# Kernel tuning notes

Hardware: AMD Instinct MI355X
Metric: run time of the kernel (lower is better)

Reference implementation:

```python
import jax, jax.numpy as jnp
import numpy as np

MAX_LEN = 2048

def setup_inputs() -> dict:
    key = jax.random.key(0)
    k1, k2, k3 = jax.random.split(key, 3)
    B, S, E, V, C = 32, 2048, 512, 50257, 2
    x = jax.random.randint(k1, (B, S), 0, V, dtype=jnp.int64)
    emb_table = jax.random.normal(k2, (V, E), dtype=jnp.float32) * 0.02
    fc_w = jax.random.normal(k3, (C, E), dtype=jnp.float32) * 0.02
    fc_b = jnp.zeros((C,), dtype=jnp.float32)
    return {"x": x, "emb_table": emb_table, "fc_w": fc_w, "fc_b": fc_b}

def reference(x, emb_table, fc_w, fc_b):
    x = x[:, :MAX_LEN]                               # [B,S]
    x_emb = emb_table[x]                             # [B,S,E]
    scores = jnp.einsum('bse,bte->bst', x_emb, x_emb)  # [B,S,S] unscaled
    attn = jax.nn.softmax(scores, axis=-1)
    attended = jnp.einsum('bst,bte->bse', attn, x_emb)  # [B,S,E]
    pooled = attended.max(axis=1)                    # pool='max' -> [B,E]
    return pooled @ fc_w.T + fc_b                    # [B,C]
```

## Files before the change

kernel.cpp:

```cpp
#include <hip/hip_runtime.h>
#include <float.h>


typedef __attribute__((ext_vector_type(8))) short short8;
typedef __attribute__((ext_vector_type(4))) float f32x4;
typedef __attribute__((ext_vector_type(16))) float f32x16;
typedef __attribute__((ext_vector_type(4))) short s16x4;

__device__ __forceinline__ short f2bf(float f) {
  unsigned u = __float_as_uint(f);
  unsigned r = (u + 0x7fffu + ((u >> 16) & 1u)) >> 16;
  return (short)r;
}
__device__ __forceinline__ unsigned ordf(float f) {
  unsigned u = __float_as_uint(f);
  return (u & 0x80000000u) ? ~u : (u | 0x80000000u);
}
__device__ __forceinline__ float unordf(unsigned e) {
  unsigned u = (e & 0x80000000u) ? (e ^ 0x80000000u) : ~e;
  return __uint_as_float(u);
}
__device__ __forceinline__ void gload16(const void* g, void* s) {
  __builtin_amdgcn_global_load_lds((const __attribute__((address_space(1))) void*)g,
                                   (__attribute__((address_space(3))) void*)s,
                                   16, 0, 0);
}
__device__ __forceinline__ unsigned pkbf(float lo, float hi) {
  unsigned r;
  asm("v_cvt_pk_bf16_f32 %0, %1, %2" : "=v"(r) : "v"(lo), "v"(hi));
  return r;
}
#define PLSWAP(a, b) asm volatile("v_permlane32_swap_b32 %0, %1" : "+v"(a), "+v"(b))

extern "C" __global__ __launch_bounds__(256)
void prep3(const int* __restrict__ xp, const float* __restrict__ emb,
           short* __restrict__ Kf, short* __restrict__ Vf) {
  __shared__ __align__(16) short ls[32 * 520];
  const int t = threadIdx.x, kt = blockIdx.x, b = blockIdx.y;
  {
    const int r = t >> 3, seg = t & 7;
    const float* src = emb + (long)xp[b * 2048 + kt * 32 + r] * 512 + seg * 64;
    short* ldst = ls + r * 520 + seg * 64;
#pragma unroll
    for (int i = 0; i < 8; ++i) {
      float4 fa = *(const float4*)(src + i * 8);
      float4 fb = *(const float4*)(src + i * 8 + 4);
      short8 v = { f2bf(fa.x), f2bf(fa.y), f2bf(fa.z), f2bf(fa.w),
                   f2bf(fb.x), f2bf(fb.y), f2bf(fb.z), f2bf(fb.w) };
      *(short8*)(ldst + i * 8) = v;
    }
  }
  __syncthreads();
#pragma unroll
  for (int rr = 0; rr < 8; ++rr) {
    int j = rr * 256 + t;
    int s = j >> 6, l = j & 63;
    int q32 = l & 31, hi = l >> 5;
    short8 v = *(const short8*)(ls + q32 * 520 + s * 16 + hi * 8);
    *(short8*)(Kf + ((long)(b * 2048 + kt * 32 + s) * 64 + l) * 8) = v;
  }
#pragma unroll
  for (int rr = 0; rr < 8; ++rr) {
    int j = rr * 256 + t;
    int eb = j >> 7, ks2 = (j >> 6) & 1, l = j & 63;
    int e32 = l & 31, hi = l >> 5;
    const short* colp = ls + (ks2 * 16 + hi * 8) * 520 + eb * 32 + e32;
    short8 v = { colp[0], colp[520], colp[1040], colp[1560],
                 colp[2080], colp[2600], colp[3120], colp[3640] };
    *(short8*)(Vf + ((long)(b * 2048 + eb * 128 + kt * 2 + ks2) * 64 + l) * 8) = v;
  }
}

extern "C" __global__ __launch_bounds__(512, 2)
void attn5(const short* __restrict__ Kf, const short* __restrict__ Vf,
           unsigned* __restrict__ pooled) {
  __shared__ __align__(16) uint4 lq4[64 * 64];
  __shared__ __align__(16) uint4 lp4[2][32 * 64];
  __shared__ float lsm[512];

  const int t = threadIdx.x, l = t & 63, w = t >> 6;
  const int n = blockIdx.x;
  const int b = (n & 7) + ((n >> 8) << 3);
  const int qt = (n >> 3) & 31;
  const int q32 = l & 31, hi = l >> 5;
  const short* lqs = (const short*)lq4;

  {
    const short* src = Kf + (long)(b * 2048 + qt * 64) * 512;
#pragma unroll
    for (int i = 0; i < 8; ++i) {
      int sw = i * 512 + w * 64;
      gload16(src + (long)(sw + l) * 8, lq4 + sw);
    }
  }

  const short* kp0 = Kf + ((long)(b * 2048 + w * 32) * 64 + l) * 8;
  const short* vp0 = Vf + ((long)(b * 2048 + (2 * w) * 128) * 64 + l) * 8;

#define LOADK(dst, base, sb)                                                  \
  {                                                                           \
    _Pragma("unroll") for (int i = 0; i < 8; ++i)                             \
        dst[i] = *(const short8*)((base) + ((sb) * 8 + i) * 512);             \
  }
#define MFMAK(src, sb)                                                        \
  {                                                                           \
    _Pragma("unroll") for (int i = 0; i < 8; ++i) {                           \
      int s = (sb) * 8 + i;                                                   \
      short8 qv0 = *(const short8*)(lqs + (s * 64 + l) * 8);                  \
      short8 qv1 = *(const short8*)(lqs + ((32 + s) * 64 + l) * 8);           \
      S0 = __builtin_amdgcn_mfma_f32_32x32x16_bf16(src[i], qv0, S0, 0, 0, 0); \
      S1 = __builtin_amdgcn_mfma_f32_32x32x16_bf16(src[i], qv1, S1, 0, 0, 0); \
    }                                                                         \
  }

  short8 kA[8], kB[8];
  LOADK(kA, kp0, 0)
  LOADK(kB, kp0, 1)
  __syncthreads();

  f32x16 acc[2][2];
#pragma unroll
  for (int eg = 0; eg < 2; ++eg)
#pragma unroll
    for (int qg = 0; qg < 2; ++qg)
#pragma unroll
      for (int r = 0; r < 16; ++r) acc[eg][qg][r] = 0.f;
  float lr0 = 0.f, lr1 = 0.f;
  int buf = 0;

  for (int kt = 0; kt < 8; ++kt) {
    const short* kp = kp0 + (long)(kt * 256) * 512;
    f32x16 S0, S1;
#pragma unroll
    for (int r = 0; r < 16; ++r) { S0[r] = 0.f; S1[r] = 0.f; }
    __builtin_amdgcn_s_setprio(1);
    MFMAK(kA, 0)
    __builtin_amdgcn_s_setprio(0);
    LOADK(kA, kp, 2)
    __builtin_amdgcn_s_setprio(1);
    MFMAK(kB, 1)
    __builtin_amdgcn_s_setprio(0);
    LOADK(kB, kp, 3)
    __builtin_amdgcn_s_setprio(1);
    MFMAK(kA, 2)
    MFMAK(kB, 3)
    __builtin_amdgcn_s_setprio(0);

    float ps0 = 0.f, ps1 = 0.f;
#pragma unroll
    for (int r = 0; r < 16; ++r) {
      S0[r] = __expf(S0[r]); ps0 += S0[r];
      S1[r] = __expf(S1[r]); ps1 += S1[r];
    }
    lr0 += ps0; lr1 += ps1;

    const short* vp = vp0 + (long)(kt * 16) * 512;
    short8 vb[8];
#pragma unroll
    for (int ks = 0; ks < 4; ++ks) {
      vb[2 * ks]     = *(const short8*)(vp + ks * 512);
      vb[2 * ks + 1] = *(const short8*)(vp + 128 * 512 + ks * 512);
    }
    if (kt < 7) {
      const short* kp2 = kp0 + (long)((kt + 1) * 256) * 512;
      LOADK(kA, kp2, 0)
      LOADK(kB, kp2, 1)
    }

    {
      unsigned a0 = pkbf(S0[0], S0[1]),   c0 = pkbf(S0[4], S0[5]);   PLSWAP(a0, c0);
      unsigned a1 = pkbf(S0[2], S0[3]),   c1 = pkbf(S0[6], S0[7]);   PLSWAP(a1, c1);
      unsigned a2 = pkbf(S0[8], S0[9]),   c2 = pkbf(S0[12], S0[13]); PLSWAP(a2, c2);
      unsigned a3 = pkbf(S0[10], S0[11]), c3 = pkbf(S0[14], S0[15]); PLSWAP(a3, c3);
      lp4[buf][(4 * w + 0) * 64 + l] = (uint4){a0, a1, c0, c1};
      lp4[buf][(4 * w + 2) * 64 + l] = (uint4){a2, a3, c2, c3};
      unsigned d0 = pkbf(S1[0], S1[1]),   e0 = pkbf(S1[4], S1[5]);   PLSWAP(d0, e0);
      unsigned d1 = pkbf(S1[2], S1[3]),   e1 = pkbf(S1[6], S1[7]);   PLSWAP(d1, e1);
      unsigned d2 = pkbf(S1[8], S1[9]),   e2 = pkbf(S1[12], S1[13]); PLSWAP(d2, e2);
      unsigned d3 = pkbf(S1[10], S1[11]), e3 = pkbf(S1[14], S1[15]); PLSWAP(d3, e3);
      lp4[buf][(4 * w + 1) * 64 + l] = (uint4){d0, d1, e0, e1};
      lp4[buf][(4 * w + 3) * 64 + l] = (uint4){d2, d3, e2, e3};
    }
    asm volatile("s_waitcnt lgkmcnt(0)" ::: "memory");
    __builtin_amdgcn_s_barrier();

    const short* lps = (const short*)lp4[buf];
#pragma unroll
    for (int ks = 0; ks < 16; ++ks) {
      short8 v0 = vb[(ks & 3) * 2];
      short8 v1 = vb[(ks & 3) * 2 + 1];
      short8 pf0 = *(const short8*)(lps + ((ks * 2 + 0) * 64 + l) * 8);
      short8 pf1 = *(const short8*)(lps + ((ks * 2 + 1) * 64 + l) * 8);
      __builtin_amdgcn_s_setprio(1);
      acc[0][0] = __builtin_amdgcn_mfma_f32_32x32x16_bf16(v0, pf0, acc[0][0], 0, 0, 0);
      acc[0][1] = __builtin_amdgcn_mfma_f32_32x32x16_bf16(v0, pf1, acc[0][1], 0, 0, 0);
      acc[1][0] = __builtin_amdgcn_mfma_f32_32x32x16_bf16(v1, pf0, acc[1][0], 0, 0, 0);
      acc[1][1] = __builtin_amdgcn_mfma_f32_32x32x16_bf16(v1, pf1, acc[1][1], 0, 0, 0);
      __builtin_amdgcn_s_setprio(0);
      if (ks < 12) {
        vb[(ks & 3) * 2]     = *(const short8*)(vp + (ks + 4) * 512);
        vb[(ks & 3) * 2 + 1] = *(const short8*)(vp + 128 * 512 + (ks + 4) * 512);
      }
    }
    buf ^= 1;
  }

  lr0 += __shfl_xor(lr0, 32, 64);
  lr1 += __shfl_xor(lr1, 32, 64);
  __syncthreads();
  if (l < 32) {
    lsm[w * 32 + l] = lr0;
    lsm[256 + w * 32 + l] = lr1;
  }
  __syncthreads();
  float lt0 = lsm[q32], lt1 = lsm[256 + q32];
#pragma unroll
  for (int kg = 1; kg < 8; ++kg) {
    lt0 += lsm[kg * 32 + q32];
    lt1 += lsm[256 + kg * 32 + q32];
  }
  float ri0 = 1.0f / lt0, ri1 = 1.0f / lt1;
#pragma unroll
  for (int eg = 0; eg < 2; ++eg)
#pragma unroll
    for (int r = 0; r < 16; ++r) {
      float v = fmaxf(acc[eg][0][r] * ri0, acc[eg][1][r] * ri1);
      v = fmaxf(v, __shfl_xor(v, 1, 64));
      v = fmaxf(v, __shfl_xor(v, 2, 64));
      v = fmaxf(v, __shfl_xor(v, 4, 64));
      v = fmaxf(v, __shfl_xor(v, 8, 64));
      v = fmaxf(v, __shfl_xor(v, 16, 64));
      if (q32 == 0) {
        int e = (2 * w + eg) * 32 + (r & 3) + 8 * (r >> 2) + 4 * hi;
        atomicMax(&pooled[b * 512 + e], ordf(v));
      }
    }
}

#define LDKp 520
#define LDVp 40
#define LDPp 40
extern "C" __global__ __launch_bounds__(256, 2)
void attn_fb(const int* __restrict__ xp, const float* __restrict__ emb,
             unsigned* __restrict__ pooled) {
  __shared__ __align__(16) short lds_k[32 * LDKp];
  __shared__ __align__(16) short lds_vt[512 * LDVp];
  __shared__ __align__(16) short lds_p[64 * LDPp];
  const int t = threadIdx.x, l = t & 63, w = t >> 6;
  const int b = blockIdx.y;
  const int q0 = blockIdx.x * 64;
  const int L = l & 15, g = l >> 4;
  short8 qf[16];
  {
    int qq = q0 + w * 16 + L;
    const float* qrow = emb + (long)xp[b * 2048 + qq] * 512;
#pragma unroll
    for (int ec = 0; ec < 16; ++ec) {
      int e0 = ec * 32 + 8 * g;
      float4 fa = *(const float4*)(qrow + e0);
      float4 fb = *(const float4*)(qrow + e0 + 4);
      short8 v = { f2bf(fa.x), f2bf(fa.y), f2bf(fa.z), f2bf(fa.w),
                   f2bf(fb.x), f2bf(fb.y), f2bf(fb.z), f2bf(fb.w) };
      qf[ec] = v;
    }
  }
  f32x4 acc[32];
#pragma unroll
  for (int nt = 0; nt < 32; ++nt) acc[nt] = (f32x4){0.f, 0.f, 0.f, 0.f};
  float mrun[4] = {-FLT_MAX, -FLT_MAX, -FLT_MAX, -FLT_MAX};
  float lrun[4] = {0.f, 0.f, 0.f, 0.f};
  for (int kt = 0; kt < 64; ++kt) {
    __syncthreads();
    if (t < 128) {
#pragma unroll 4
      for (int i = 0; i < 32; ++i) {
        const float* krow = emb + (long)xp[b * 2048 + kt * 32 + i] * 512;
        float4 f = *(const float4*)(krow + 4 * t);
        s16x4 v = { f2bf(f.x), f2bf(f.y), f2bf(f.z), f2bf(f.w) };
        *(s16x4*)&lds_k[i * LDKp + 4 * t] = v;
      }
    } else {
      const int u = t - 128, lane_ = u & 63, half = u >> 6;
#pragma unroll 2
      for (int kq = 0; kq < 8; ++kq) {
        const int kbase = b * 2048 + kt * 32 + kq * 4;
        const float* r0 = emb + (long)xp[kbase + 0] * 512;
        const float* r1 = emb + (long)xp[kbase + 1] * 512;
        const float* r2 = emb + (long)xp[kbase + 2] * 512;
        const float* r3 = emb + (long)xp[kbase + 3] * 512;
#pragma unroll
        for (int seg = 0; seg < 4; ++seg) {
          int e = lane_ + 64 * (seg + 4 * half);
          s16x4 v = { f2bf(r0[e]), f2bf(r1[e]), f2bf(r2[e]), f2bf(r3[e]) };
          *(s16x4*)&lds_vt[e * LDVp + 4 * kq] = v;
        }
      }
    }
    __syncthreads();
    f32x4 s0 = {0.f, 0.f, 0.f, 0.f}, s1 = {0.f, 0.f, 0.f, 0.f};
#pragma unroll
    for (int ec = 0; ec < 16; ++ec) {
      short8 k0 = *(const short8*)&lds_k[L * LDKp + ec * 32 + 8 * g];
      short8 k1 = *(const short8*)&lds_k[(L + 16) * LDKp + ec * 32 + 8 * g];
      s0 = __builtin_amdgcn_mfma_f32_16x16x32_bf16(qf[ec], k0, s0, 0, 0, 0);
      s1 = __builtin_amdgcn_mfma_f32_16x16x32_bf16(qf[ec], k1, s1, 0, 0, 0);
    }
    float p0[4], p1[4], sc[4];
#pragma unroll
    for (int r = 0; r < 4; ++r) {
      float v = fmaxf(s0[r], s1[r]);
      v = fmaxf(v, __shfl_xor(v, 1, 64));
      v = fmaxf(v, __shfl_xor(v, 2, 64));
      v = fmaxf(v, __shfl_xor(v, 4, 64));
      v = fmaxf(v, __shfl_xor(v, 8, 64));
      float nm = fmaxf(mrun[r], v);
      sc[r] = expf(mrun[r] - nm);
      p0[r] = expf(s0[r] - nm);
      p1[r] = expf(s1[r] - nm);
      float rs = p0[r] + p1[r];
      rs += __shfl_xor(rs, 1, 64);
      rs += __shfl_xor(rs, 2, 64);
      rs += __shfl_xor(rs, 4, 64);
      rs += __shfl_xor(rs, 8, 64);
      lrun[r] = lrun[r] * sc[r] + rs;
      mrun[r] = nm;
    }
    if (__any(sc[0] < 1.f || sc[1] < 1.f || sc[2] < 1.f || sc[3] < 1.f)) {
      f32x4 sv = { sc[0], sc[1], sc[2], sc[3] };
#pragma unroll
      for (int nt = 0; nt < 32; ++nt) acc[nt] *= sv;
    }
#pragma unroll
    for (int r = 0; r < 4; ++r) {
      int row = w * 16 + g * 4 + r;
      lds_p[row * LDPp + L]      = f2bf(p0[r]);
      lds_p[row * LDPp + 16 + L] = f2bf(p1[r]);
    }
    asm volatile("s_waitcnt lgkmcnt(0)" ::: "memory");
    short8 pf = *(const short8*)&lds_p[(w * 16 + L) * LDPp + 8 * g];
#pragma unroll
    for (int nt = 0; nt < 32; ++nt) {
      short8 vf = *(const short8*)&lds_vt[(nt * 16 + L) * LDVp + 8 * g];
      acc[nt] = __builtin_amdgcn_mfma_f32_16x16x32_bf16(pf, vf, acc[nt], 0, 0, 0);
    }
  }
  __syncthreads();
  float inv[4];
#pragma unroll
  for (int r = 0; r < 4; ++r) inv[r] = 1.f / lrun[r];
  float* rbuf = (float*)lds_k;
#pragma unroll
  for (int nt = 0; nt < 32; ++nt) {
    f32x4 a = acc[nt];
    float c = fmaxf(fmaxf(a[0] * inv[0], a[1] * inv[1]),
                    fmaxf(a[2] * inv[2], a[3] * inv[3]));
    c = fmaxf(c, __shfl_xor(c, 16, 64));
    c = fmaxf(c, __shfl_xor(c, 32, 64));
    if (g == 0) rbuf[w * 512 + nt * 16 + L] = c;
  }
  __syncthreads();
  for (int j = t; j < 512; j += 256) {
    float v = fmaxf(fmaxf(rbuf[j], rbuf[512 + j]),
                    fmaxf(rbuf[1024 + j], rbuf[1536 + j]));
    atomicMax(&pooled[b * 512 + j], ordf(v));
  }
}

extern "C" __global__ void fc_small(const unsigned* __restrict__ pooled,
                                    const float* __restrict__ fw,
                                    const float* __restrict__ fb,
                                    float* __restrict__ out) {
  int t = threadIdx.x;
  if (t >= 64) return;
  int bb = t >> 1, c = t & 1;
  float s = fb[c];
  for (int e = 0; e < 512; ++e)
    s += unordf(pooled[bb * 512 + e]) * fw[c * 512 + e];
  out[t] = s;
}

extern "C" void kernel_launch(void* const* d_in, const int* in_sizes, int n_in,
                              void* d_out, int out_size, void* d_ws, size_t ws_size,
                              hipStream_t stream) {
  const int* xp    = (const int*)d_in[0];
  const float* emb = (const float*)d_in[1];
  const float* fw  = (const float*)d_in[2];
  const float* fb  = (const float*)d_in[3];
  unsigned* pooled = (unsigned*)d_ws;

  hipMemsetAsync(pooled, 0, 32 * 512 * sizeof(unsigned), stream);

  const size_t need = 65536ull + 2ull * 33554432ull * sizeof(short);
  if (ws_size >= need) {
    short* Kff = (short*)((char*)d_ws + 65536);
    short* Vff = Kff + 33554432;
    prep3<<<dim3(64, 32), 256, 0, stream>>>(xp, emb, Kff, Vff);
    attn5<<<dim3(1024), 512, 0, stream>>>(Kff, Vff, pooled);
  } else {
    attn_fb<<<dim3(32, 32), 256, 0, stream>>>(xp, emb, pooled);
  }
  fc_small<<<1, 64, 0, stream>>>(pooled, fw, fb, (float*)d_out);
}
```

Baseline: 344.6 us.

## Warp-specialize attention: producer waves compute QK softmax, consumer waves do PV

Splits the 8 waves of the attention block into 4 producer waves that compute the QK^T scores, exponentiate and write bf16 probabilities to double-buffered LDS, and 4 consumer waves that run the PV MFMAs and the max-pooling. The goal is to overlap the score and exp work with the PV matrix multiplies across waves instead of serialising them within each wave. In exchange the producers and consumers must stay in lockstep through matched s_barrier counts, each wave holds more registers (acc[4][2] on consumers), and the MFMA work is now split unevenly between the two roles. An unused attn6 variant that never writes pooled is also left in the file.

After: 357.8 us. 1.04x slower.

```diff
diff --git a/kernel.cpp b/kernel.cpp
--- a/kernel.cpp
+++ b/kernel.cpp
@@ -72,11 +72,11 @@
 }
 
 extern "C" __global__ __launch_bounds__(512, 2)
-void attn5(const short* __restrict__ Kf, const short* __restrict__ Vf,
+void attn6(const short* __restrict__ Kf, const short* __restrict__ Vf,
            unsigned* __restrict__ pooled) {
   __shared__ __align__(16) uint4 lq4[64 * 64];
   __shared__ __align__(16) uint4 lp4[2][32 * 64];
-  __shared__ float lsm[512];
+  __shared__ float lsm[256];
 
   const int t = threadIdx.x, l = t & 63, w = t >> 6;
   const int n = blockIdx.x;
@@ -94,147 +94,282 @@
     }
   }
 
-  const short* kp0 = Kf + ((long)(b * 2048 + w * 32) * 64 + l) * 8;
-  const short* vp0 = Vf + ((long)(b * 2048 + (2 * w) * 128) * 64 + l) * 8;
-
-#define LOADK(dst, base, sb)                                                  \
+#define PLOADP(d0, d1, p0, p1, off)                                           \
   {                                                                           \
-    _Pragma("unroll") for (int i = 0; i < 8; ++i)                             \
-        dst[i] = *(const short8*)((base) + ((sb) * 8 + i) * 512);             \
-  }
-#define MFMAK(src, sb)                                                        \
+    _Pragma("unroll") for (int i = 0; i < 4; ++i) {                           \
+      d0[i] = *(const short8*)((p0) + (off) + i * 512);                       \
+      d1[i] = *(const short8*)((p1) + (off) + i * 512);                       \
+    }                                                                         \
+  }
+#define PMFMA(s0_, s1_, ch)                                                   \
   {                                                                           \
-    _Pragma("unroll") for (int i = 0; i < 8; ++i) {                           \
-      int s = (sb) * 8 + i;                                                   \
+    __builtin_amdgcn_s_setprio(1);                                            \
+    _Pragma("unroll") for (int i = 0; i < 4; ++i) {                           \
+      int s = (ch) * 4 + i;                                                   \
       short8 qv0 = *(const short8*)(lqs + (s * 64 + l) * 8);                  \
       short8 qv1 = *(const short8*)(lqs + ((32 + s) * 64 + l) * 8);           \
-      S0 = __builtin_amdgcn_mfma_f32_32x32x16_bf16(src[i], qv0, S0, 0, 0, 0); \
-      S1 = __builtin_amdgcn_mfma_f32_32x32x16_bf16(src[i], qv1, S1, 0, 0, 0); \
+      S00 = __builtin_amdgcn_mfma_f32_32x32x16_bf16(s0_[i], qv0, S00, 0, 0, 0); \
+      S01 = __builtin_amdgcn_mfma_f32_32x32x16_bf16(s0_[i], qv1, S01, 0, 0, 0); \
+      S10 = __builtin_amdgcn_mfma_f32_32x32x16_bf16(s1_[i], qv0, S10, 0, 0, 0); \
+      S11 = __builtin_amdgcn_mfma_f32_32x32x16_bf16(s1_[i], qv1, S11, 0, 0, 0); \
     }                                                                         \
-  }
-
-  short8 kA[8], kB[8];
-  LOADK(kA, kp0, 0)
-  LOADK(kB, kp0, 1)
+    __builtin_amdgcn_s_setprio(0);                                            \
+  }
+#define PACK(Sq0, Sq1, sb, buf)                                               \
+  {                                                                           \
+    unsigned a0 = pkbf(Sq0[0], Sq0[1]),  c0 = pkbf(Sq0[4], Sq0[5]);  PLSWAP(a0, c0); \
+    unsigned a1 = pkbf(Sq0[2], Sq0[3]),  c1 = pkbf(Sq0[6], Sq0[7]);  PLSWAP(a1, c1); \
+    unsigned a2 = pkbf(Sq0[8], Sq0[9]),  c2 = pkbf(Sq0[12], Sq0[13]); PLSWAP(a2, c2); \
+    unsigned a3 = pkbf(Sq0[10], Sq0[11]), c3 = pkbf(Sq0[14], Sq0[15]); PLSWAP(a3, c3); \
+    lp4[buf][((sb) + 0) * 64 + l] = (uint4){a0, a1, c0, c1};                  \
+    lp4[buf][((sb) + 2) * 64 + l] = (uint4){a2, a3, c2, c3};                  \
+    unsigned d0 = pkbf(Sq1[0], Sq1[1]),  e0 = pkbf(Sq1[4], Sq1[5]);  PLSWAP(d0, e0); \
+    unsigned d1 = pkbf(Sq1[2], Sq1[3]),  e1 = pkbf(Sq1[6], Sq1[7]);  PLSWAP(d1, e1); \
+    unsigned d2 = pkbf(Sq1[8], Sq1[9]),  e2 = pkbf(Sq1[12], Sq1[13]); PLSWAP(d2, e2); \
+    unsigned d3 = pkbf(Sq1[10], Sq1[11]), e3 = pkbf(Sq1[14], Sq1[15]); PLSWAP(d3, e3); \
+    lp4[buf][((sb) + 1) * 64 + l] = (uint4){d0, d1, e0, e1};                  \
+    lp4[buf][((sb) + 3) * 64 + l] = (uint4){d2, d3, e2, e3};                  \
+  }
+
+  if (w < 4) {
+    const short* kb0 = Kf + (long)(b * 2048 + (2 * w + 0) * 32) * 512 + l * 8;
+    const short* kb1 = Kf + (long)(b * 2048 + (2 * w + 1) * 32) * 512 + l * 8;
+    short8 kA0[4], kA1[4], kB0[4], kB1[4];
+    PLOADP(kA0, kA1, kb0, kb1, 0)
+    PLOADP(kB0, kB1, kb0, kb1, 2048)
+    float lr0 = 0.f, lr1 = 0.f;
+    __syncthreads();
+
+    for (int kt = 0; kt < 8; ++kt) {
+      const short* kp0 = kb0 + (long)kt * 131072;
+      const short* kp1 = kb1 + (long)kt * 131072;
+      const long nxt = (kt < 7) ? 131072 : 0;
+      f32x16 S00, S01, S10, S11;
+#pragma unroll
+      for (int r = 0; r < 16; ++r) { S00[r] = 0.f; S01[r] = 0.f; S10[r] = 0.f; S11[r] = 0.f; }
+      PMFMA(kA0, kA1, 0) PLOADP(kA0, kA1, kp0, kp1, 2 * 2048)
+      PMFMA(kB0, kB1, 1) PLOADP(kB0, kB1, kp0, kp1, 3 * 2048)
+      PMFMA(kA0, kA1, 2) PLOADP(kA0, kA1, kp0, kp1, 4 * 2048)
+      PMFMA(kB0, kB1, 3) PLOADP(kB0, kB1, kp0, kp1, 5 * 2048)
+      PMFMA(kA0, kA1, 4) PLOADP(kA0, kA1, kp0, kp1, 6 * 2048)
+      PMFMA(kB0, kB1, 5) PLOADP(kB0, kB1, kp0, kp1, 7 * 2048)
+      PMFMA(kA0, kA1, 6) PLOADP(kA0, kA1, kp0, kp1, nxt)
+      PMFMA(kB0, kB1, 7) PLOADP(kB0, kB1, kp0, kp1, nxt + 2048)
+
+      float ps0 = 0.f, ps1 = 0.f;
+#pragma unroll
+      for (int r = 0; r < 16; ++r) {
+        S00[r] = __expf(S00[r]); ps0 += S00[r];
+        S01[r] = __expf(S01[r]); ps1 += S01[r];
+        S10[r] = __expf(S10[r]); ps0 += S10[r];
+        S11[r] = __expf(S11[r]); ps1 += S11[r];
+      }
+      lr0 += ps0; lr1 += ps1;
+
+      const int buf = kt & 1;
+      PACK(S00, S01, 8 * w, buf)
+      PACK(S10, S11, 8 * w + 4, buf)
+      asm volatile("s_waitcnt lgkmcnt(0)" ::: "memory");
+      __builtin_amdgcn_s_barrier();
+    }
+    __builtin_amdgcn_s_barrier();
+
+    lr0 += __shfl_xor(lr0, 32, 64);
+    lr1 += __shfl_xor(lr1, 32, 64);
+    if (l < 32) {
+      lsm[w * 32 + l] = lr0;
+      lsm[128 + w * 32 + l] = lr1;
+    }
+  } else {
+    const int wc = w - 4;
+    const short* vp0 = Vf + (long)(b * 2048 + (4 * wc + 0) * 128) * 512 + l * 8;
+    const short* vp1 = Vf + (long)(b * 2048 + (4 * wc + 1) * 128) * 512 + l * 8;
+    const short* vp2 = Vf + (long)(b * 2048 + (4 * wc + 2) * 128) * 512 + l * 8;
+    const short* vp3 = Vf + (long)(b * 2048 + (4 * wc + 3) * 128) * 512 + l * 8;
+    f32x16 acc[4][2];
+#pragma unroll
+    for (int g = 0; g < 4; ++g)
+#pragma unroll
+      for (int qg = 0; qg < 2; ++qg)
+#pragma unroll
+        for (int r = 0; r < 16; ++r) acc[g][qg][r] = 0.f;
+    short8 vbA[4], vbB[4];
+    vbA[0] = *(const short8*)(vp0); vbA[1] = *(const short8*)(vp1);
+    vbA[2] = *(const short8*)(vp2); vbA[3] = *(const short8*)(vp3);
+    vbB[0] = *(const short8*)(vp0 + 512); vbB[1] = *(const short8*)(vp1 + 512);
+    vbB[2] = *(const short8*)(vp2 + 512); vbB[3] = *(const short8*)(vp3 + 512);
+    __syncthreads();
+    __builtin_amdgcn_s_barrier();
+
+#define CSTEP(ks_, ring)                                                      \
+  {                                                                           \
+    short8 pf0 = *(const short8*)(lps + ((2 * (ks_)) * 64 + l) * 8);          \
+    short8 pf1 = *(const short8*)(lps + ((2 * (ks_) + 1) * 64 + l) * 8);      \
+    __builtin_amdgcn_s_setprio(1);                                            \
+    _Pragma("unroll") for (int g = 0; g < 4; ++g) {                           \
+      acc[g][0] = __builtin_amdgcn_mfma_f32_32x32x16_bf16(ring[g], pf0, acc[g][0], 0, 0, 0); \
+      acc[g][1] = __builtin_amdgcn_mfma_f32_32x32x16_bf16(ring[g], pf1, acc[g][1], 0, 0, 0); \
+    }                                                                         \
+    __builtin_amdgcn_s_setprio(0);                                            \
+    {                                                                         \
+      const int nk = (ksg0 + (ks_) + 2) & 127;                                \
+      ring[0] = *(const short8*)(vp0 + (long)nk * 512);                       \
+      ring[1] = *(const short8*)(vp1 + (long)nk * 512);                       \
+      ring[2] = *(const short8*)(vp2 + (long)nk * 512);                       \
+      ring[3] = *(const short8*)(vp3 + (long)nk * 512);                       \
+    }                                                                         \
+  }
+
+    for (int kt = 1; kt <= 8; ++kt) {
+      const short* lps = (const short*)lp4[(kt - 1) & 1];
+      const int ksg0 = (kt - 1) * 16;
+#pragma unroll
+      for (int ks2 = 0; ks2 < 8; ++ks2) {
+        CSTEP(2 * ks2, vbA)
+        CSTEP(2 * ks2 + 1, vbB)
+      }
+      __builtin_amdgcn_s_barrier();
+    }
+
+    (void)0;
+  }
   __syncthreads();
 
-  f32x16 acc[2][2];
-#pragma unroll
-  for (int eg = 0; eg < 2; ++eg)
-#pragma unroll
-    for (int qg = 0; qg < 2; ++qg)
-#pragma unroll
-      for (int r = 0; r < 16; ++r) acc[eg][qg][r] = 0.f;
-  float lr0 = 0.f, lr1 = 0.f;
-  int buf = 0;
-
-  for (int kt = 0; kt < 8; ++kt) {
-    const short* kp = kp0 + (long)(kt * 256) * 512;
-    f32x16 S0, S1;
-#pragma unroll
-    for (int r = 0; r < 16; ++r) { S0[r] = 0.f; S1[r] = 0.f; }
-    __builtin_amdgcn_s_setprio(1);
-    MFMAK(kA, 0)
-    __builtin_amdgcn_s_setprio(0);
-    LOADK(kA, kp, 2)
-    __builtin_amdgcn_s_setprio(1);
-    MFMAK(kB, 1)
-    __builtin_amdgcn_s_setprio(0);
-    LOADK(kB, kp, 3)
-    __builtin_amdgcn_s_setprio(1);
-    MFMAK(kA, 2)
-    MFMAK(kB, 3)
-    __builtin_amdgcn_s_setprio(0);
-
-    float ps0 = 0.f, ps1 = 0.f;
-#pragma unroll
-    for (int r = 0; r < 16; ++r) {
-      S0[r] = __expf(S0[r]); ps0 += S0[r];
-      S1[r] = __expf(S1[r]); ps1 += S1[r];
-    }
-    lr0 += ps0; lr1 += ps1;
-
-    const short* vp = vp0 + (long)(kt * 16) * 512;
-    short8 vb[8];
-#pragma unroll
-    for (int ks = 0; ks < 4; ++ks) {
-      vb[2 * ks]     = *(const short8*)(vp + ks * 512);
-      vb[2 * ks + 1] = *(const short8*)(vp + 128 * 512 + ks * 512);
-    }
-    if (kt < 7) {
-      const short* kp2 = kp0 + (long)((kt + 1) * 256) * 512;
-      LOADK(kA, kp2, 0)
-      LOADK(kB, kp2, 1)
-    }
-
-    {
-      unsigned a0 = pkbf(S0[0], S0[1]),   c0 = pkbf(S0[4], S0[5]);   PLSWAP(a0, c0);
-      unsigned a1 = pkbf(S0[2], S0[3]),   c1 = pkbf(S0[6], S0[7]);   PLSWAP(a1, c1);
-      unsigned a2 = pkbf(S0[8], S0[9]),   c2 = pkbf(S0[12], S0[13]); PLSWAP(a2, c2);
-      unsigned a3 = pkbf(S0[10], S0[11]), c3 = pkbf(S0[14], S0[15]); PLSWAP(a3, c3);
-      lp4[buf][(4 * w + 0) * 64 + l] = (uint4){a0, a1, c0, c1};
-      lp4[buf][(4 * w + 2) * 64 + l] = (uint4){a2, a3, c2, c3};
-      unsigned d0 = pkbf(S1[0], S1[1]),   e0 = pkbf(S1[4], S1[5]);   PLSWAP(d0, e0);
-      unsigned d1 = pkbf(S1[2], S1[3]),   e1 = pkbf(S1[6], S1[7]);   PLSWAP(d1, e1);
-      unsigned d2 = pkbf(S1[8], S1[9]),   e2 = pkbf(S1[12], S1[13]); PLSWAP(d2, e2);
-      unsigned d3 = pkbf(S1[10], S1[11]), e3 = pkbf(S1[14], S1[15]); PLSWAP(d3, e3);
-      lp4[buf][(4 * w + 1) * 64 + l] = (uint4){d0, d1, e0, e1};
-      lp4[buf][(4 * w + 3) * 64 + l] = (uint4){d2, d3, e2, e3};
-    }
-    asm volatile("s_waitcnt lgkmcnt(0)" ::: "memory");
+  if (w >= 4) {
+    const int wc = w - 4;
+    float lt0 = lsm[q32] + lsm[32 + q32] + lsm[64 + q32] + lsm[96 + q32];
+    float lt1 = lsm[128 + q32] + lsm[160 + q32] + lsm[192 + q32] + lsm[224 + q32];
+    float ri0 = 1.0f / lt0, ri1 = 1.0f / lt1;
+    (void)ri0; (void)ri1; (void)wc;
+  }
+}
+
+
+extern "C" __global__ __launch_bounds__(512, 2)
+void attn6b(const short* __restrict__ Kf, const short* __restrict__ Vf,
+            unsigned* __restrict__ pooled) {
+  __shared__ __align__(16) uint4 lq4[64 * 64];
+  __shared__ __align__(16) uint4 lp4[2][32 * 64];
+  __shared__ float lsm[256];
+
+  const int t = threadIdx.x, l = t & 63, w = t >> 6;
+  const int n = blockIdx.x;
+  const int b = (n & 7) + ((n >> 8) << 3);
+  const int qt = (n >> 3) & 31;
+  const int q32 = l & 31, hi = l >> 5;
+  const short* lqs = (const short*)lq4;
+
+  {
+    const short* src = Kf + (long)(b * 2048 + qt * 64) * 512;
+#pragma unroll
+    for (int i = 0; i < 8; ++i) {
+      int sw = i * 512 + w * 64;
+      gload16(src + (long)(sw + l) * 8, lq4 + sw);
+    }
+  }
+
+  if (w < 4) {
+    const short* kb0 = Kf + (long)(b * 2048 + (2 * w + 0) * 32) * 512 + l * 8;
+    const short* kb1 = Kf + (long)(b * 2048 + (2 * w + 1) * 32) * 512 + l * 8;
+    short8 kA0[4], kA1[4], kB0[4], kB1[4];
+    PLOADP(kA0, kA1, kb0, kb1, 0)
+    PLOADP(kB0, kB1, kb0, kb1, 2048)
+    float lr0 = 0.f, lr1 = 0.f;
+    __syncthreads();
+
+    for (int kt = 0; kt < 8; ++kt) {
+      const short* kp0 = kb0 + (long)kt * 131072;
+      const short* kp1 = kb1 + (long)kt * 131072;
+      const long nxt = (kt < 7) ? 131072 : 0;
+      f32x16 S00, S01, S10, S11;
+#pragma unroll
+      for (int r = 0; r < 16; ++r) { S00[r] = 0.f; S01[r] = 0.f; S10[r] = 0.f; S11[r] = 0.f; }
+      PMFMA(kA0, kA1, 0) PLOADP(kA0, kA1, kp0, kp1, 2 * 2048)
+      PMFMA(kB0, kB1, 1) PLOADP(kB0, kB1, kp0, kp1, 3 * 2048)
+      PMFMA(kA0, kA1, 2) PLOADP(kA0, kA1, kp0, kp1, 4 * 2048)
+      PMFMA(kB0, kB1, 3) PLOADP(kB0, kB1, kp0, kp1, 5 * 2048)
+      PMFMA(kA0, kA1, 4) PLOADP(kA0, kA1, kp0, kp1, 6 * 2048)
+      PMFMA(kB0, kB1, 5) PLOADP(kB0, kB1, kp0, kp1, 7 * 2048)
+      PMFMA(kA0, kA1, 6) PLOADP(kA0, kA1, kp0, kp1, nxt)
+      PMFMA(kB0, kB1, 7) PLOADP(kB0, kB1, kp0, kp1, nxt + 2048)
+
+      float ps0 = 0.f, ps1 = 0.f;
+#pragma unroll
+      for (int r = 0; r < 16; ++r) {
+        S00[r] = __expf(S00[r]); ps0 += S00[r];
+        S01[r] = __expf(S01[r]); ps1 += S01[r];
+        S10[r] = __expf(S10[r]); ps0 += S10[r];
+        S11[r] = __expf(S11[r]); ps1 += S11[r];
+      }
+      lr0 += ps0; lr1 += ps1;
+
+      const int buf = kt & 1;
+      PACK(S00, S01, 8 * w, buf)
+      PACK(S10, S11, 8 * w + 4, buf)
+      asm volatile("s_waitcnt lgkmcnt(0)" ::: "memory");
+      __builtin_amdgcn_s_barrier();
+    }
     __builtin_amdgcn_s_barrier();
 
-    const short* lps = (const short*)lp4[buf];
-#pragma unroll
-    for (int ks = 0; ks < 16; ++ks) {
-      short8 v0 = vb[(ks & 3) * 2];
-      short8 v1 = vb[(ks & 3) * 2 + 1];
-      short8 pf0 = *(const short8*)(lps + ((ks * 2 + 0) * 64 + l) * 8);
-      short8 pf1 = *(const short8*)(lps + ((ks * 2 + 1) * 64 + l) * 8);
-      __builtin_amdgcn_s_setprio(1);
-      acc[0][0] = __builtin_amdgcn_mfma_f32_32x32x16_bf16(v0, pf0, acc[0][0], 0, 0, 0);
-      acc[0][1] = __builtin_amdgcn_mfma_f32_32x32x16_bf16(v0, pf1, acc[0][1], 0, 0, 0);
-      acc[1][0] = __builtin_amdgcn_mfma_f32_32x32x16_bf16(v1, pf0, acc[1][0], 0, 0, 0);
-      acc[1][1] = __builtin_amdgcn_mfma_f32_32x32x16_bf16(v1, pf1, acc[1][1], 0, 0, 0);
-      __builtin_amdgcn_s_setprio(0);
-      if (ks < 12) {
-        vb[(ks & 3) * 2]     = *(const short8*)(vp + (ks + 4) * 512);
-        vb[(ks & 3) * 2 + 1] = *(const short8*)(vp + 128 * 512 + (ks + 4) * 512);
-      }
-    }
-    buf ^= 1;
-  }
-
-  lr0 += __shfl_xor(lr0, 32, 64);
-  lr1 += __shfl_xor(lr1, 32, 64);
-  __syncthreads();
-  if (l < 32) {
-    lsm[w * 32 + l] = lr0;
-    lsm[256 + w * 32 + l] = lr1;
-  }
-  __syncthreads();
-  float lt0 = lsm[q32], lt1 = lsm[256 + q32];
-#pragma unroll
-  for (int kg = 1; kg < 8; ++kg) {
-    lt0 += lsm[kg * 32 + q32];
-    lt1 += lsm[256 + kg * 32 + q32];
-  }
-  float ri0 = 1.0f / lt0, ri1 = 1.0f / lt1;
-#pragma unroll
-  for (int eg = 0; eg < 2; ++eg)
-#pragma unroll
-    for (int r = 0; r < 16; ++r) {
-      float v = fmaxf(acc[eg][0][r] * ri0, acc[eg][1][r] * ri1);
-      v = fmaxf(v, __shfl_xor(v, 1, 64));
-      v = fmaxf(v, __shfl_xor(v, 2, 64));
-      v = fmaxf(v, __shfl_xor(v, 4, 64));
-      v = fmaxf(v, __shfl_xor(v, 8, 64));
-      v = fmaxf(v, __shfl_xor(v, 16, 64));
-      if (q32 == 0) {
-        int e = (2 * w + eg) * 32 + (r & 3) + 8 * (r >> 2) + 4 * hi;
-        atomicMax(&pooled[b * 512 + e], ordf(v));
-      }
-    }
+    lr0 += __shfl_xor(lr0, 32, 64);
+    lr1 += __shfl_xor(lr1, 32, 64);
+    if (l < 32) {
+      lsm[w * 32 + l] = lr0;
+      lsm[128 + w * 32 + l] = lr1;
+    }
+    __syncthreads();
+  } else {
+    const int wc = w - 4;
+    const short* vp0 = Vf + (long)(b * 2048 + (4 * wc + 0) * 128) * 512 + l * 8;
+    const short* vp1 = Vf + (long)(b * 2048 + (4 * wc + 1) * 128) * 512 + l * 8;
+    const short* vp2 = Vf + (long)(b * 2048 + (4 * wc + 2) * 128) * 512 + l * 8;
+    const short* vp3 = Vf + (long)(b * 2048 + (4 * wc + 3) * 128) * 512 + l * 8;
+    f32x16 acc[4][2];
+#pragma unroll
+    for (int g = 0; g < 4; ++g)
+#pragma unroll
+      for (int qg = 0; qg < 2; ++qg)
+#pragma unroll
+        for (int r = 0; r < 16; ++r) acc[g][qg][r] = 0.f;
+    short8 vbA[4], vbB[4];
+    vbA[0] = *(const short8*)(vp0); vbA[1] = *(const short8*)(vp1);
+    vbA[2] = *(const short8*)(vp2); vbA[3] = *(const short8*)(vp3);
+    vbB[0] = *(const short8*)(vp0 + 512); vbB[1] = *(const short8*)(vp1 + 512);
+    vbB[2] = *(const short8*)(vp2 + 512); vbB[3] = *(const short8*)(vp3 + 512);
+    __syncthreads();
+    __builtin_amdgcn_s_barrier();
+
+    for (int kt = 1; kt <= 8; ++kt) {
+      const short* lps = (const short*)lp4[(kt - 1) & 1];
+      const int ksg0 = (kt - 1) * 16;
+#pragma unroll
+      for (int ks2 = 0; ks2 < 8; ++ks2) {
+        CSTEP(2 * ks2, vbA)
+        CSTEP(2 * ks2 + 1, vbB)
+      }
+      __builtin_amdgcn_s_barrier();
+    }
+    __syncthreads();
+
+    float lt0 = lsm[q32] + lsm[32 + q32] + lsm[64 + q32] + lsm[96 + q32];
+    float lt1 = lsm[128 + q32] + lsm[160 + q32] + lsm[192 + q32] + lsm[224 + q32];
+    float ri0 = 1.0f / lt0, ri1 = 1.0f / lt1;
+#pragma unroll
+    for (int g = 0; g < 4; ++g)
+#pragma unroll
+      for (int r = 0; r < 16; ++r) {
+        float v = fmaxf(acc[g][0][r] * ri0, acc[g][1][r] * ri1);
+        v = fmaxf(v, __shfl_xor(v, 1, 64));
+        v = fmaxf(v, __shfl_xor(v, 2, 64));
+        v = fmaxf(v, __shfl_xor(v, 4, 64));
+        v = fmaxf(v, __shfl_xor(v, 8, 64));
+        v = fmaxf(v, __shfl_xor(v, 16, 64));
+        if (q32 == 0) {
+          int e = 128 * wc + 32 * g + (r & 3) + 8 * (r >> 2) + 4 * hi;
+          atomicMax(&pooled[b * 512 + e], ordf(v));
+        }
+      }
+  }
 }
 
 #define LDKp 520
@@ -395,7 +530,7 @@
     short* Kff = (short*)((char*)d_ws + 65536);
     short* Vff = Kff + 33554432;
     prep3<<<dim3(64, 32), 256, 0, stream>>>(xp, emb, Kff, Vff);
-    attn5<<<dim3(1024), 512, 0, stream>>>(Kff, Vff, pooled);
+    attn6b<<<dim3(1024), 512, 0, stream>>>(Kff, Vff, pooled);
   } else {
     attn_fb<<<dim3(32, 32), 256, 0, stream>>>(xp, emb, pooled);
   }
```

## Quantize Q/K to FP8 e4m3 and compute scores with FP8 MFMA

Applied to the files above, without the earlier changes.

The prep kernel now emits K (which also serves as Q) in FP8 e4m3 with a new packed layout, and the attention kernel computes QK^T with 32x32x16 fp8 MFMA instead of bf16. This halves K/Q memory traffic and LDS footprint and uses the higher-throughput FP8 matrix path. The K prefetch schedule is simplified so whole tiles are loaded ahead. The risk is reduced score precision: embeddings are ~0.02 scale, so many values fall into e4m3 subnormals or flush to zero, which could change the softmax output.

Result: faster. 310.7 us (-9.8%).

```diff
diff --git a/kernel.cpp b/kernel.cpp
--- a/kernel.cpp
+++ b/kernel.cpp
@@ -12,6 +12,31 @@
   unsigned r = (u + 0x7fffu + ((u >> 16) & 1u)) >> 16;
   return (short)r;
 }
+__device__ __forceinline__ float bf2f(short s) {
+  return __uint_as_float(((unsigned)(unsigned short)s) << 16);
+}
+__device__ __forceinline__ unsigned f2e4m3(float f) {
+  unsigned u = __float_as_uint(f);
+  unsigned s = (u >> 31) << 7;
+  int exp = (int)((u >> 23) & 0xff) - 127;
+  unsigned m = (u & 0x7fffff) | 0x800000;
+  if (exp < -10) return s;
+  int shift = 20, e4 = 0;
+  if (exp >= -6) e4 = exp + 7;
+  else shift += (-6 - exp);
+  unsigned keep = m >> shift;
+  unsigned rem = m & ((1u << shift) - 1u);
+  unsigned half = 1u << (shift - 1);
+  keep += (rem > half || (rem == half && (keep & 1)));
+  unsigned out;
+  if (e4 > 0) {
+    if (keep >= 16) { keep >>= 1; e4++; }
+    out = ((unsigned)e4 << 3) | (keep & 7);
+  } else {
+    out = (keep >= 8) ? ((1u << 3) | (keep & 7)) : keep;
+  }
+  return s | out;
+}
 __device__ __forceinline__ unsigned ordf(float f) {
   unsigned u = __float_as_uint(f);
   return (u & 0x80000000u) ? ~u : (u | 0x80000000u);
@@ -31,10 +56,13 @@
   return r;
 }
 #define PLSWAP(a, b) asm volatile("v_permlane32_swap_b32 %0, %1" : "+v"(a), "+v"(b))
+__device__ __forceinline__ long long mklong(unsigned lo, unsigned hi) {
+  return (long long)((((unsigned long long)hi) << 32) | lo);
+}
 
 extern "C" __global__ __launch_bounds__(256)
-void prep3(const int* __restrict__ xp, const float* __restrict__ emb,
-           short* __restrict__ Kf, short* __restrict__ Vf) {
+void prep4(const int* __restrict__ xp, const float* __restrict__ emb,
+           unsigned char* __restrict__ Kf8, short* __restrict__ Vf) {
   __shared__ __align__(16) short ls[32 * 520];
   const int t = threadIdx.x, kt = blockIdx.x, b = blockIdx.y;
   {
@@ -51,13 +79,28 @@
     }
   }
   __syncthreads();
-#pragma unroll
-  for (int rr = 0; rr < 8; ++rr) {
-    int j = rr * 256 + t;
-    int s = j >> 6, l = j & 63;
-    int q32 = l & 31, hi = l >> 5;
-    short8 v = *(const short8*)(ls + q32 * 520 + s * 16 + hi * 8);
-    *(short8*)(Kf + ((long)(b * 2048 + kt * 32 + s) * 64 + l) * 8) = v;
+  {
+    const long chunkK = ((long)b * 64 + kt) * 16384;
+#pragma unroll
+    for (int i = 0; i < 4; ++i) {
+      int j = t * 4 + i;
+      int sp = j >> 6, lj = j & 63;
+      int keyl = lj & 31, hi2 = lj >> 5;
+      const short* row = ls + keyl * 520 + 8 * hi2;
+      unsigned dw[4];
+#pragma unroll
+      for (int c2 = 0; c2 < 4; ++c2) {
+        unsigned d = 0;
+#pragma unroll
+        for (int bb2 = 0; bb2 < 4; ++bb2) {
+          int c = c2 * 4 + bb2;
+          int e = 16 * (2 * sp + (c >> 3)) + (c & 7);
+          d |= f2e4m3(bf2f(row[e])) << (8 * bb2);
+        }
+        dw[c2] = d;
+      }
+      *(uint4*)(Kf8 + chunkK + (long)j * 16) = (uint4){dw[0], dw[1], dw[2], dw[3]};
+    }
   }
 #pragma unroll
   for (int rr = 0; rr < 8; ++rr) {
@@ -72,9 +115,9 @@
 }
 
 extern "C" __global__ __launch_bounds__(512, 2)
-void attn5(const short* __restrict__ Kf, const short* __restrict__ Vf,
+void attn7(const unsigned char* __restrict__ Kf8, const short* __restrict__ Vf,
            unsigned* __restrict__ pooled) {
-  __shared__ __align__(16) uint4 lq4[64 * 64];
+  __shared__ __align__(16) uint4 lq8[32 * 64];
   __shared__ __align__(16) uint4 lp4[2][32 * 64];
   __shared__ float lsm[512];
 
@@ -83,39 +126,39 @@
   const int b = (n & 7) + ((n >> 8) << 3);
   const int qt = (n >> 3) & 31;
   const int q32 = l & 31, hi = l >> 5;
-  const short* lqs = (const short*)lq4;
 
   {
-    const short* src = Kf + (long)(b * 2048 + qt * 64) * 512;
-#pragma unroll
-    for (int i = 0; i < 8; ++i) {
+    const unsigned char* src = Kf8 + ((long)b * 64 + 2 * qt) * 16384;
+#pragma unroll
+    for (int i = 0; i < 4; ++i) {
       int sw = i * 512 + w * 64;
-      gload16(src + (long)(sw + l) * 8, lq4 + sw);
-    }
-  }
-
-  const short* kp0 = Kf + ((long)(b * 2048 + w * 32) * 64 + l) * 8;
+      gload16(src + (long)(sw + l) * 16, lq8 + sw);
+    }
+  }
+
+  const unsigned char* kc0 = Kf8 + ((long)b * 64 + w) * 16384 + (long)l * 16;
   const short* vp0 = Vf + ((long)(b * 2048 + (2 * w) * 128) * 64 + l) * 8;
 
-#define LOADK(dst, base, sb)                                                  \
+#define LOADK8(dst, base, half)                                               \
   {                                                                           \
     _Pragma("unroll") for (int i = 0; i < 8; ++i)                             \
-        dst[i] = *(const short8*)((base) + ((sb) * 8 + i) * 512);             \
-  }
-#define MFMAK(src, sb)                                                        \
+        dst[i] = *(const uint4*)((base) + ((half) * 8 + i) * 1024);           \
+  }
+#define QK8(kv, sp)                                                           \
   {                                                                           \
-    _Pragma("unroll") for (int i = 0; i < 8; ++i) {                           \
-      int s = (sb) * 8 + i;                                                   \
-      short8 qv0 = *(const short8*)(lqs + (s * 64 + l) * 8);                  \
-      short8 qv1 = *(const short8*)(lqs + ((32 + s) * 64 + l) * 8);           \
-      S0 = __builtin_amdgcn_mfma_f32_32x32x16_bf16(src[i], qv0, S0, 0, 0, 0); \
-      S1 = __builtin_amdgcn_mfma_f32_32x32x16_bf16(src[i], qv1, S1, 0, 0, 0); \
-    }                                                                         \
-  }
-
-  short8 kA[8], kB[8];
-  LOADK(kA, kp0, 0)
-  LOADK(kB, kp0, 1)
+    long long ak0 = mklong(kv.x, kv.y);                                       \
+    long long ak1 = mklong(kv.z, kv.w);                                       \
+    uint4 qa = lq8[(sp) * 64 + l];                                            \
+    uint4 qb = lq8[(16 + (sp)) * 64 + l];                                     \
+    S0 = __builtin_amdgcn_mfma_f32_32x32x16_fp8_fp8(ak0, mklong(qa.x, qa.y), S0, 0, 0, 0); \
+    S1 = __builtin_amdgcn_mfma_f32_32x32x16_fp8_fp8(ak0, mklong(qb.x, qb.y), S1, 0, 0, 0); \
+    S0 = __builtin_amdgcn_mfma_f32_32x32x16_fp8_fp8(ak1, mklong(qa.z, qa.w), S0, 0, 0, 0); \
+    S1 = __builtin_amdgcn_mfma_f32_32x32x16_fp8_fp8(ak1, mklong(qb.z, qb.w), S1, 0, 0, 0); \
+  }
+
+  uint4 kA[8], kB[8];
+  LOADK8(kA, kc0, 0)
+  LOADK8(kB, kc0, 1)
   __syncthreads();
 
   f32x16 acc[2][2];
@@ -129,21 +172,14 @@
   int buf = 0;
 
   for (int kt = 0; kt < 8; ++kt) {
-    const short* kp = kp0 + (long)(kt * 256) * 512;
     f32x16 S0, S1;
 #pragma unroll
     for (int r = 0; r < 16; ++r) { S0[r] = 0.f; S1[r] = 0.f; }
     __builtin_amdgcn_s_setprio(1);
-    MFMAK(kA, 0)
-    __builtin_amdgcn_s_setprio(0);
-    LOADK(kA, kp, 2)
-    __builtin_amdgcn_s_setprio(1);
-    MFMAK(kB, 1)
-    __builtin_amdgcn_s_setprio(0);
-    LOADK(kB, kp, 3)
-    __builtin_amdgcn_s_setprio(1);
-    MFMAK(kA, 2)
-    MFMAK(kB, 3)
+#pragma unroll
+    for (int sp = 0; sp < 8; ++sp) QK8(kA[sp], sp)
+#pragma unroll
+    for (int sp = 0; sp < 8; ++sp) QK8(kB[sp], 8 + sp)
     __builtin_amdgcn_s_setprio(0);
 
     float ps0 = 0.f, ps1 = 0.f;
@@ -161,10 +197,11 @@
       vb[2 * ks]     = *(const short8*)(vp + ks * 512);
       vb[2 * ks + 1] = *(const short8*)(vp + 128 * 512 + ks * 512);
     }
-    if (kt < 7) {
-      const short* kp2 = kp0 + (long)((kt + 1) * 256) * 512;
-      LOADK(kA, kp2, 0)
-      LOADK(kB, kp2, 1)
+    {
+      const int nkt = (kt < 7) ? kt + 1 : 7;
+      const unsigned char* kcn = kc0 + (long)nkt * 131072;
+      LOADK8(kA, kcn, 0)
+      LOADK8(kB, kcn, 1)
     }
 
     {
@@ -390,12 +427,12 @@
 
   hipMemsetAsync(pooled, 0, 32 * 512 * sizeof(unsigned), stream);
 
-  const size_t need = 65536ull + 2ull * 33554432ull * sizeof(short);
+  const size_t need = 65536ull + 33554432ull + 2ull * 33554432ull * sizeof(short);
   if (ws_size >= need) {
-    short* Kff = (short*)((char*)d_ws + 65536);
-    short* Vff = Kff + 33554432;
-    prep3<<<dim3(64, 32), 256, 0, stream>>>(xp, emb, Kff, Vff);
-    attn5<<<dim3(1024), 512, 0, stream>>>(Kff, Vff, pooled);
+    unsigned char* Kf8 = (unsigned char*)d_ws + 65536;
+    short* Vff = (short*)(Kf8 + 33554432);
+    prep4<<<dim3(64, 32), 256, 0, stream>>>(xp, emb, Kf8, Vff);
+    attn7<<<dim3(1024), 512, 0, stream>>>(Kf8, Vff, pooled);
   } else {
     attn_fb<<<dim3(32, 32), 256, 0, stream>>>(xp, emb, pooled);
   }
```
